# Kernel tuning notes

Measured on AMD Instinct MI355X. Metric: run time of the kernel, lower is better.

## Reference

```python
import jax, jax.numpy as jnp
import numpy as np

D = 2048
H = 16
HD = D // H
B = 2
T = 2048
EPS = 1e-5


def _gated(x, W, b, Wg, bg):
    # MoEGatedLinear: linear output elementwise-gated by sigmoid of a linear router
    return (x @ W.T + b) * jax.nn.sigmoid(x @ Wg.T + bg)


def _ln(x, g, b):
    m = jnp.mean(x, axis=-1, keepdims=True)
    v = jnp.mean((x - m) ** 2, axis=-1, keepdims=True)
    return (x - m) * jax.lax.rsqrt(v + EPS) * g + b


def setup_inputs() -> dict:
    key = jax.random.key(0)
    ks = jax.random.split(key, 16)
    w = lambda k, o, i: (jax.random.normal(k, (o, i), jnp.float32) * 0.02)
    inp = {"x": jax.random.normal(ks[0], (B, T, D), jnp.float32)}
    for i, n in enumerate(["q", "k", "v", "o"]):
        inp[f"W_{n}"] = w(jax.random.fold_in(ks[1], i), D, D)
        inp[f"b_{n}"] = jnp.zeros((D,), jnp.float32)
        inp[f"Wg_{n}"] = w(jax.random.fold_in(ks[2], i), D, D)
        inp[f"bg_{n}"] = jnp.zeros((D,), jnp.float32)
    inp["W_in"] = w(ks[3], 4 * D, D)
    inp["b_in"] = jnp.zeros((4 * D,), jnp.float32)
    inp["Wg_in"] = w(ks[4], 4 * D, D)
    inp["bg_in"] = jnp.zeros((4 * D,), jnp.float32)
    inp["W_out"] = w(ks[5], D, 4 * D)
    inp["b_out"] = jnp.zeros((D,), jnp.float32)
    inp["Wg_out"] = w(ks[6], D, 4 * D)
    inp["bg_out"] = jnp.zeros((D,), jnp.float32)
    inp["ln1_g"] = jnp.ones((D,), jnp.float32)
    inp["ln1_b"] = jnp.zeros((D,), jnp.float32)
    inp["ln2_g"] = jnp.ones((D,), jnp.float32)
    inp["ln2_b"] = jnp.zeros((D,), jnp.float32)
    return inp


def reference(x, W_q, b_q, Wg_q, bg_q, W_k, b_k, Wg_k, bg_k, W_v, b_v, Wg_v, bg_v,
              W_o, b_o, Wg_o, bg_o, W_in, b_in, Wg_in, bg_in, W_out, b_out, Wg_out, bg_out,
              ln1_g, ln1_b, ln2_g, ln2_b):
    Bb, Tt, C = x.shape
    resid = x
    h = _ln(x, ln1_g, ln1_b)
    q = _gated(h, W_q, b_q, Wg_q, bg_q).reshape(Bb, Tt, H, HD).transpose(0, 2, 1, 3)
    k = _gated(h, W_k, b_k, Wg_k, bg_k).reshape(Bb, Tt, H, HD).transpose(0, 2, 1, 3)
    v = _gated(h, W_v, b_v, Wg_v, bg_v).reshape(Bb, Tt, H, HD).transpose(0, 2, 1, 3)
    att = jnp.einsum('bhqd,bhkd->bhqk', q, k) * (1.0 / np.sqrt(HD))
    att = jax.nn.softmax(att, axis=-1)  # full (no causal mask) per source
    y = jnp.einsum('bhqk,bhkd->bhqd', att, v)
    y = y.transpose(0, 2, 1, 3).reshape(Bb, Tt, C)
    y = _gated(y, W_o, b_o, Wg_o, bg_o)
    x = resid + y
    resid = x
    h = _ln(x, ln2_g, ln2_b)
    h = _gated(h, W_in, b_in, Wg_in, bg_in)
    h = jax.nn.gelu(h, approximate=False)  # torch nn.GELU default = exact erf
    h = _gated(h, W_out, b_out, Wg_out, bg_out)
    return resid + h
```

## Files before the change

kernel.cpp:

```cpp
#include <hip/hip_runtime.h>
#include <cstdint>
#include <cmath>

#define DD 2048
#define TT 2048
#define HH 16
#define HDD 128
#define MROWS 4096

typedef __attribute__((ext_vector_type(8))) short s16x8;
typedef __attribute__((ext_vector_type(4))) float f32x4;

typedef const __attribute__((address_space(1))) void gvoid;
typedef __attribute__((address_space(3))) void lvoid;

__device__ __forceinline__ void async_cp16(const void* g, void* l) {
    __builtin_amdgcn_global_load_lds((gvoid*)g, (lvoid*)l, 16, 0, 0);
}

__device__ __forceinline__ unsigned short f2bf(float f) {
    unsigned int u = __float_as_uint(f);
    u += 0x7fffu + ((u >> 16) & 1u);
    return (unsigned short)(u >> 16);
}

__device__ __forceinline__ void store4bf(unsigned short* p, float a, float b, float c, float d) {
    union { unsigned short u[4]; uint2 v; } x;
    x.u[0] = f2bf(a); x.u[1] = f2bf(b); x.u[2] = f2bf(c); x.u[3] = f2bf(d);
    *(uint2*)p = x.v;
}

__global__ __launch_bounds__(256) void cvt_bf16(const float* __restrict__ src,
                                                unsigned short* __restrict__ dst, int n4) {
    int i = blockIdx.x * 256 + threadIdx.x;
    if (i < n4) {
        float4 v = ((const float4*)src)[i];
        store4bf(dst + (size_t)i * 4, v.x, v.y, v.z, v.w);
    }
}

__global__ __launch_bounds__(256) void ln_bf16(const float* __restrict__ x,
                                               const float* __restrict__ gg,
                                               const float* __restrict__ bb,
                                               unsigned short* __restrict__ out) {
    __shared__ float red[8];
    const int row = blockIdx.x, t = threadIdx.x;
    const float* xr = x + (size_t)row * DD;
    float4 a = ((const float4*)xr)[t];
    float4 c = ((const float4*)xr)[t + 256];
    float s = a.x + a.y + a.z + a.w + c.x + c.y + c.z + c.w;
    float q = a.x*a.x + a.y*a.y + a.z*a.z + a.w*a.w + c.x*c.x + c.y*c.y + c.z*c.z + c.w*c.w;
    #pragma unroll
    for (int m = 1; m < 64; m <<= 1) { s += __shfl_xor(s, m); q += __shfl_xor(q, m); }
    if ((t & 63) == 0) { red[t >> 6] = s; red[4 + (t >> 6)] = q; }
    __syncthreads();
    s = red[0] + red[1] + red[2] + red[3];
    q = red[4] + red[5] + red[6] + red[7];
    float mean = s * (1.f / DD);
    float var = q * (1.f / DD) - mean * mean;
    float rstd = rsqrtf(var + 1e-5f);
    float4 g1 = ((const float4*)gg)[t], b1 = ((const float4*)bb)[t];
    float4 g2 = ((const float4*)gg)[t + 256], b2 = ((const float4*)bb)[t + 256];
    unsigned short* orow = out + (size_t)row * DD;
    store4bf(orow + 4 * t,
             (a.x - mean) * rstd * g1.x + b1.x, (a.y - mean) * rstd * g1.y + b1.y,
             (a.z - mean) * rstd * g1.z + b1.z, (a.w - mean) * rstd * g1.w + b1.w);
    store4bf(orow + 1024 + 4 * t,
             (c.x - mean) * rstd * g2.x + b2.x, (c.y - mean) * rstd * g2.y + b2.y,
             (c.z - mean) * rstd * g2.z + b2.z, (c.w - mean) * rstd * g2.w + b2.w);
}

template <int EPI>
__global__ __launch_bounds__(256, 3) void gemm_gated(
        const unsigned short* __restrict__ A, const unsigned short* __restrict__ W,
        const unsigned short* __restrict__ Wg, const float* __restrict__ bias,
        const float* __restrict__ biasg, const float* __restrict__ resid,
        void* __restrict__ outp, int M, int N, int K) {
    __shared__ unsigned short lds_[(EPI == 1) ? 8704 : 8192];
    const int t = threadIdx.x, lane = t & 63, wv = t >> 6;

    const int nbg = gridDim.x;
    int pid = blockIdx.y * nbg + blockIdx.x;
    int npg = 8 * nbg;
    int grp = pid / npg;
    int loc = pid - grp * npg;
    const int m0 = (grp * 8 + (loc & 7)) * 128;
    const int n0 = (loc >> 3) * 64;

    const int srow = t >> 2;
    const int scol = (t & 3) * 8;
    const unsigned short* gA = A + (size_t)(m0 + srow) * K + scol;
    const unsigned short* gB = W + (size_t)(n0 + srow) * K + scol;
    const unsigned short* gBg = Wg + (size_t)(n0 + srow) * K + scol;

    const int mw = (wv >> 1) * 64, nw = (wv & 1) * 32;
    const int fr = lane & 15, fg = lane >> 4, fk = fg * 8;

    f32x4 zero4 = {0.f, 0.f, 0.f, 0.f};
    f32x4 acc[4][2], accg[4][2];
    #pragma unroll
    for (int i = 0; i < 4; i++)
        #pragma unroll
        for (int j = 0; j < 2; j++) { acc[i][j] = zero4; accg[i][j] = zero4; }

    for (int k0 = 0; k0 < K; k0 += 32) {
        async_cp16(gA + k0, lds_ + t * 8);
        async_cp16(gA + (size_t)64 * K + k0, lds_ + 2048 + t * 8);
        async_cp16(gB + k0, lds_ + 4096 + t * 8);
        async_cp16(gBg + k0, lds_ + 6144 + t * 8);
        __syncthreads();
        s16x8 af[4], bf_[2], bg_[2];
        #pragma unroll
        for (int i = 0; i < 4; i++)
            af[i] = *(const s16x8*)(lds_ + (mw + i * 16 + fr) * 32 + fk);
        #pragma unroll
        for (int j = 0; j < 2; j++) {
            bf_[j] = *(const s16x8*)(lds_ + 4096 + (nw + j * 16 + fr) * 32 + fk);
            bg_[j] = *(const s16x8*)(lds_ + 6144 + (nw + j * 16 + fr) * 32 + fk);
        }
        #pragma unroll
        for (int i = 0; i < 4; i++)
            #pragma unroll
            for (int j = 0; j < 2; j++) {
                acc[i][j] = __builtin_amdgcn_mfma_f32_16x16x32_bf16(af[i], bf_[j], acc[i][j], 0, 0, 0);
                accg[i][j] = __builtin_amdgcn_mfma_f32_16x16x32_bf16(af[i], bg_[j], accg[i][j], 0, 0, 0);
            }
        __syncthreads();
    }

    #pragma unroll
    for (int i = 0; i < 4; i++)
        #pragma unroll
        for (int j = 0; j < 2; j++) {
            const int n = n0 + nw + j * 16 + fr;
            const float bn = bias[n], bgn = biasg[n];
            #pragma unroll
            for (int r = 0; r < 4; r++) {
                const int m = m0 + mw + i * 16 + fg * 4 + r;
                float lin = acc[i][j][r] + bn;
                float gt = accg[i][j][r] + bgn;
                float gv = lin / (1.f + __expf(-gt));
                if constexpr (EPI == 0) {
                    ((unsigned short*)outp)[(size_t)m * N + n] = f2bf(gv);
                } else if constexpr (EPI == 1) {
                    lds_[(nw + j * 16 + fr) * 136 + (mw + i * 16 + fg * 4 + r)] = f2bf(gv);
                } else if constexpr (EPI == 2) {
                    ((float*)outp)[(size_t)m * N + n] = resid[(size_t)m * N + n] + gv;
                } else {
                    float ge = 0.5f * gv * (1.f + erff(gv * 0.70710678118f));
                    ((unsigned short*)outp)[(size_t)m * N + n] = f2bf(ge);
                }
            }
        }

    if constexpr (EPI == 1) {
        __syncthreads();
        const int n_l = t >> 2;
        const int ch = t & 3;
        const unsigned short* src = lds_ + n_l * 136 + ch * 32;
        const int hglob = n0 + n_l;
        const int b_ = m0 >> 11;
        const int tseq = (m0 & 2047) + ch * 32;
        unsigned short* dst = (unsigned short*)outp +
            (((size_t)b_ * HH + (hglob >> 7)) * HDD + (hglob & 127)) * TT + tseq;
        #pragma unroll
        for (int c = 0; c < 4; c++)
            *(uint4*)(dst + c * 8) = *(const uint4*)(src + c * 8);
    }
}

__global__ __launch_bounds__(256, 4) void attn_flash2(const unsigned short* __restrict__ Q,
                                                      const unsigned short* __restrict__ Kb,
                                                      const unsigned short* __restrict__ VT,
                                                      unsigned short* __restrict__ Y) {
    __shared__ unsigned short sK[64 * 128];
    __shared__ unsigned short sV[128 * 64];
    __shared__ unsigned short sP[4 * 1024];
    const int t = threadIdx.x, lane = t & 63, wv = t >> 6;
    const int bx = blockIdx.x;
    const int qblk = bx & 31;
    const int h = (bx >> 5) & 15;
    const int b = bx >> 9;
    const int q0 = qblk * 64 + wv * 16;
    const int fr = lane & 15, fg = lane >> 4;

    s16x8 qf[4];
    const unsigned short* qbase = Q + ((size_t)(b * TT + q0 + fr)) * DD + h * HDD + fg * 8;
    #pragma unroll
    for (int s = 0; s < 4; s++) qf[s] = *(const s16x8*)(qbase + s * 32);

    const unsigned short* kSrc[4];
    const unsigned short* vSrc[4];
    #pragma unroll
    for (int r = 0; r < 4; r++) {
        int R = r * 16 + (t >> 4);
        int c = (t & 15) ^ ((t >> 4) & 15);
        kSrc[r] = Kb + (size_t)(b * TT + R) * DD + h * HDD + c * 8;
        int hd = r * 32 + (t >> 3);
        int cv = (t & 7) ^ ((t >> 3) & 7);
        vSrc[r] = VT + ((size_t)((b * HH + h) * HDD + hd)) * TT + cv * 8;
    }
    unsigned short* sPw = sP + wv * 1024;

    f32x4 zero4 = {0.f, 0.f, 0.f, 0.f};
    f32x4 o[8];
    #pragma unroll
    for (int jo = 0; jo < 8; jo++) o[jo] = zero4;
    float Mx[4], L[4];
    #pragma unroll
    for (int r = 0; r < 4; r++) { Mx[r] = -1e30f; L[r] = 0.f; }
    const float scale = 0.08838834764831845f;

    for (int tk0 = 0; tk0 < TT; tk0 += 64) {
        #pragma unroll
        for (int r = 0; r < 4; r++) {
            async_cp16(kSrc[r] + (size_t)tk0 * DD, sK + r * 2048 + t * 8);
            async_cp16(vSrc[r] + tk0, sV + r * 2048 + t * 8);
        }
        __syncthreads();

        f32x4 sac[4];
        #pragma unroll
        for (int j = 0; j < 4; j++) sac[j] = zero4;
        #pragma unroll
        for (int j = 0; j < 4; j++)
            #pragma unroll
            for (int s = 0; s < 4; s++) {
                s16x8 kf = *(const s16x8*)(sK + (j * 16 + fr) * 128 + (((s * 4 + fg) ^ fr) * 8));
                sac[j] = __builtin_amdgcn_mfma_f32_16x16x32_bf16(qf[s], kf, sac[j], 0, 0, 0);
            }

        float alpha[4];
        #pragma unroll
        for (int j = 0; j < 4; j++)
            #pragma unroll
            for (int r = 0; r < 4; r++) sac[j][r] *= scale;
        #pragma unroll
        for (int r = 0; r < 4; r++) {
            float mx = fmaxf(fmaxf(sac[0][r], sac[1][r]), fmaxf(sac[2][r], sac[3][r]));
            mx = fmaxf(mx, __shfl_xor(mx, 1));
            mx = fmaxf(mx, __shfl_xor(mx, 2));
            mx = fmaxf(mx, __shfl_xor(mx, 4));
            mx = fmaxf(mx, __shfl_xor(mx, 8));
            float mnew = fmaxf(Mx[r], mx);
            alpha[r] = __expf(Mx[r] - mnew);
            Mx[r] = mnew;
        }
        float rs[4] = {0.f, 0.f, 0.f, 0.f};
        #pragma unroll
        for (int j = 0; j < 4; j++)
            #pragma unroll
            for (int r = 0; r < 4; r++) {
                float p = __expf(sac[j][r] - Mx[r]);
                rs[r] += p;
                int qr = fg * 4 + r;
                int cc = (j * 2 + (fr >> 3)) ^ (qr & 7);
                sPw[qr * 64 + cc * 8 + (fr & 7)] = f2bf(p);
            }
        #pragma unroll
        for (int r = 0; r < 4; r++) {
            float tsum = rs[r];
            tsum += __shfl_xor(tsum, 1);
            tsum += __shfl_xor(tsum, 2);
            tsum += __shfl_xor(tsum, 4);
            tsum += __shfl_xor(tsum, 8);
            L[r] = L[r] * alpha[r] + tsum;
        }
        #pragma unroll
        for (int jo = 0; jo < 8; jo++)
            #pragma unroll
            for (int r = 0; r < 4; r++) o[jo][r] *= alpha[r];

        s16x8 pa[2];
        #pragma unroll
        for (int ks = 0; ks < 2; ks++)
            pa[ks] = *(const s16x8*)(sPw + fr * 64 + (((ks * 4 + fg) ^ (fr & 7)) * 8));
        #pragma unroll
        for (int jo = 0; jo < 8; jo++)
            #pragma unroll
            for (int ks = 0; ks < 2; ks++) {
                s16x8 vf = *(const s16x8*)(sV + (jo * 16 + fr) * 64 + (((ks * 4 + fg) ^ (fr & 7)) * 8));
                o[jo] = __builtin_amdgcn_mfma_f32_16x16x32_bf16(pa[ks], vf, o[jo], 0, 0, 0);
            }
        __syncthreads();
    }
    float Linv[4];
    #pragma unroll
    for (int r = 0; r < 4; r++) Linv[r] = 1.f / L[r];
    #pragma unroll
    for (int jo = 0; jo < 8; jo++)
        #pragma unroll
        for (int r = 0; r < 4; r++) {
            float val = o[jo][r] * Linv[r];
            Y[((size_t)(b * TT + q0 + fg * 4 + r)) * DD + h * HDD + jo * 16 + fr] = f2bf(val);
        }
}

extern "C" void kernel_launch(void* const* d_in, const int* in_sizes, int n_in,
                              void* d_out, int out_size, void* d_ws, size_t ws_size,
                              hipStream_t stream) {
    const float* x = (const float*)d_in[0];
    auto F = [&](int i) { return (const float*)d_in[i]; };
    char* ws = (char*)d_ws;
    const size_t MB = 1ull << 20;

    static const int widx_[12] = {1, 3, 5, 7, 9, 11, 13, 15, 17, 19, 21, 23};
    static const size_t woffMB[12] = {0, 8, 16, 24, 32, 40, 48, 56, 64, 96, 128, 160};
    unsigned short* wbf[12];
    for (int i = 0; i < 12; i++) {
        wbf[i] = (unsigned short*)(ws + woffMB[i] * MB);
        size_t n = (i < 8) ? (size_t)DD * DD : (size_t)4 * DD * DD;
        cvt_bf16<<<dim3((unsigned)(n / 4 / 256)), dim3(256), 0, stream>>>(F(widx_[i]), wbf[i], (int)(n / 4));
    }
    unsigned short* hbf = (unsigned short*)(ws + 192 * MB);
    unsigned short* qb  = (unsigned short*)(ws + 208 * MB);
    unsigned short* kb  = (unsigned short*)(ws + 224 * MB);
    unsigned short* vtb = (unsigned short*)(ws + 240 * MB);
    unsigned short* yb  = (unsigned short*)(ws + 256 * MB);
    unsigned short* ub  = (unsigned short*)(ws + 208 * MB);
    float* x1 = (float*)(ws + 272 * MB);

    ln_bf16<<<dim3(MROWS), dim3(256), 0, stream>>>(x, F(25), F(26), hbf);

    dim3 blk(256);
    gemm_gated<0><<<dim3(32, 32), blk, 0, stream>>>(hbf, wbf[0], wbf[1], F(2), F(4), nullptr, qb, MROWS, DD, DD);
    gemm_gated<0><<<dim3(32, 32), blk, 0, stream>>>(hbf, wbf[2], wbf[3], F(6), F(8), nullptr, kb, MROWS, DD, DD);
    gemm_gated<1><<<dim3(32, 32), blk, 0, stream>>>(hbf, wbf[4], wbf[5], F(10), F(12), nullptr, vtb, MROWS, DD, DD);

    attn_flash2<<<dim3(1024), blk, 0, stream>>>(qb, kb, vtb, yb);

    gemm_gated<2><<<dim3(32, 32), blk, 0, stream>>>(yb, wbf[6], wbf[7], F(14), F(16), x, x1, MROWS, DD, DD);

    ln_bf16<<<dim3(MROWS), dim3(256), 0, stream>>>(x1, F(27), F(28), hbf);

    gemm_gated<3><<<dim3(128, 32), blk, 0, stream>>>(hbf, wbf[8], wbf[9], F(18), F(20), nullptr, ub, MROWS, 4 * DD, DD);
    gemm_gated<2><<<dim3(32, 32), blk, 0, stream>>>(ub, wbf[10], wbf[11], F(22), F(24), x1, (float*)d_out, MROWS, DD, 4 * DD);
}
```

Measured before the change: 1.690 ms.

## Replace gated GEMM with 256x256 interleaved-weight pipelined 8-wave kernel

Weights W and Wg are interleaved in 16-row blocks during bf16 conversion, so a single B operand tile holds both the linear and the gate columns. The GEMM moves from 128x64 tiles with 256 threads to 256x256 tiles with 512 threads. It uses double-buffered 64-wide K steps in a swizzled LDS layout, split-phase loads overlapped with MFMA, setprio, and explicit vmcnt waits. The aim is higher arithmetic intensity and better latency hiding. The trade-offs are heavy register and LDS use (128KB LDS, occupancy 2) and fewer workgroups, which can leave CUs underfilled on the 2048-wide GEMMs (256 blocks).

```diff
diff --git a/kernel.cpp b/kernel.cpp
--- a/kernel.cpp
+++ b/kernel.cpp
@@ -30,13 +30,16 @@
     *(uint2*)p = x.v;
 }
 
-__global__ __launch_bounds__(256) void cvt_bf16(const float* __restrict__ src,
-                                                unsigned short* __restrict__ dst, int n4) {
-    int i = blockIdx.x * 256 + threadIdx.x;
-    if (i < n4) {
-        float4 v = ((const float4*)src)[i];
-        store4bf(dst + (size_t)i * 4, v.x, v.y, v.z, v.w);
-    }
+__global__ __launch_bounds__(256) void cvt_ilv(const float* __restrict__ W,
+                                               const float* __restrict__ Wg,
+                                               unsigned short* __restrict__ out, int k4shift) {
+    int g = blockIdx.x * 256 + threadIdx.x;
+    int rp = g >> k4shift;
+    int c4 = g & ((1 << k4shift) - 1);
+    int jb = rp >> 5, s = rp & 15, sel = (rp >> 4) & 1;
+    const float* src = (sel ? Wg : W) + (((size_t)(jb * 16 + s)) << (k4shift + 2)) + c4 * 4;
+    float4 v = *(const float4*)src;
+    store4bf(out + (((size_t)rp) << (k4shift + 2)) + c4 * 4, v.x, v.y, v.z, v.w);
 }
 
 __global__ __launch_bounds__(256) void ln_bf16(const float* __restrict__ x,
@@ -70,102 +73,181 @@
              (c.z - mean) * rstd * g2.z + b2.z, (c.w - mean) * rstd * g2.w + b2.w);
 }
 
+#define G8_LDA(base, iq) do { \
+    _Pragma("unroll") \
+    for (int i2_ = 0; i2_ < 4; i2_++) \
+        af[i2_] = *(const s16x8*)(lds + (base) + aRd + ((iq) * 4 + i2_) * 1024); \
+} while (0)
+#define G8_LDB(base) do { \
+    _Pragma("unroll") \
+    for (int j_ = 0; j_ < 4; j_++) \
+        bf[j_] = *(const s16x8*)(lds + (base) + bRd + j_ * 1024); \
+} while (0)
+#define G8_MMA(iq) do { \
+    __builtin_amdgcn_s_setprio(1); \
+    _Pragma("unroll") \
+    for (int i2_ = 0; i2_ < 4; i2_++) { \
+        _Pragma("unroll") \
+        for (int j_ = 0; j_ < 4; j_++) \
+            acc[(iq) * 4 + i2_][j_] = __builtin_amdgcn_mfma_f32_16x16x32_bf16( \
+                af[i2_], bf[j_], acc[(iq) * 4 + i2_][j_], 0, 0, 0); \
+    } \
+    __builtin_amdgcn_s_setprio(0); \
+} while (0)
+#define G8_BAR() __builtin_amdgcn_s_barrier()
+#define G8_SCB() __builtin_amdgcn_sched_barrier(0)
+#define G8_VM4() asm volatile("s_waitcnt vmcnt(4)" ::: "memory")
+#define G8_VM0() asm volatile("s_waitcnt vmcnt(0)" ::: "memory")
+
 template <int EPI>
-__global__ __launch_bounds__(256, 3) void gemm_gated(
-        const unsigned short* __restrict__ A, const unsigned short* __restrict__ W,
-        const unsigned short* __restrict__ Wg, const float* __restrict__ bias,
-        const float* __restrict__ biasg, const float* __restrict__ resid,
-        void* __restrict__ outp, int M, int N, int K) {
-    __shared__ unsigned short lds_[(EPI == 1) ? 8704 : 8192];
+__global__ __launch_bounds__(512, 2) void gemm_gated8(
+        const unsigned short* __restrict__ A, const unsigned short* __restrict__ Wi,
+        const float* __restrict__ bias, const float* __restrict__ biasg,
+        const float* __restrict__ resid, void* __restrict__ outp,
+        int M, int Ntrue, int K) {
+    __shared__ unsigned short lds_[65536];
+    char* lds = (char*)lds_;
     const int t = threadIdx.x, lane = t & 63, wv = t >> 6;
-
-    const int nbg = gridDim.x;
-    int pid = blockIdx.y * nbg + blockIdx.x;
-    int npg = 8 * nbg;
-    int grp = pid / npg;
-    int loc = pid - grp * npg;
-    const int m0 = (grp * 8 + (loc & 7)) * 128;
-    const int n0 = (loc >> 3) * 64;
-
-    const int srow = t >> 2;
-    const int scol = (t & 3) * 8;
-    const unsigned short* gA = A + (size_t)(m0 + srow) * K + scol;
-    const unsigned short* gB = W + (size_t)(n0 + srow) * K + scol;
-    const unsigned short* gBg = Wg + (size_t)(n0 + srow) * K + scol;
-
-    const int mw = (wv >> 1) * 64, nw = (wv & 1) * 32;
-    const int fr = lane & 15, fg = lane >> 4, fk = fg * 8;
-
+    const int fr = lane & 15, fg = lane >> 4;
+    const int wr = wv >> 2, wc = wv & 3;
+
+    const int nM = M >> 8;
+    const int nwg = gridDim.x;
+    const int pid = blockIdx.x;
+    const int swz = (pid & 7) * (nwg >> 3) + (pid >> 3);
+    const int nt = swz / nM;
+    const int mt = swz - nt * nM;
+    const int m0 = mt << 8;
+    const int np0 = nt << 8;
+
+    const unsigned short* aP[2];
+    const unsigned short* bP[2];
+    int ldst[2];
+    #pragma unroll
+    for (int l = 0; l < 2; l++) {
+        int idx = l * 512 + t;
+        int p = idx >> 3, pc = idx & 7;
+        int spc = pc ^ (p & 7);
+        int lr = 2 * p + (spc >> 2);
+        int ke = (spc & 3) * 8;
+        aP[l] = A + (size_t)(m0 + lr) * K + ke;
+        bP[l] = Wi + (size_t)(np0 + lr) * K + ke;
+        ldst[l] = idx * 16;
+    }
+    const int chR = (((fr & 1) << 2) | fg) ^ ((fr >> 1) & 7);
+    const int aRd = (wr * 64 + (fr >> 1)) * 128 + chR * 16;
+    const int bRd = (wc * 32 + (fr >> 1)) * 128 + chR * 16;
+
+    f32x4 acc[8][4];
     f32x4 zero4 = {0.f, 0.f, 0.f, 0.f};
-    f32x4 acc[4][2], accg[4][2];
-    #pragma unroll
-    for (int i = 0; i < 4; i++)
-        #pragma unroll
-        for (int j = 0; j < 2; j++) { acc[i][j] = zero4; accg[i][j] = zero4; }
-
-    for (int k0 = 0; k0 < K; k0 += 32) {
-        async_cp16(gA + k0, lds_ + t * 8);
-        async_cp16(gA + (size_t)64 * K + k0, lds_ + 2048 + t * 8);
-        async_cp16(gB + k0, lds_ + 4096 + t * 8);
-        async_cp16(gBg + k0, lds_ + 6144 + t * 8);
-        __syncthreads();
-        s16x8 af[4], bf_[2], bg_[2];
-        #pragma unroll
-        for (int i = 0; i < 4; i++)
-            af[i] = *(const s16x8*)(lds_ + (mw + i * 16 + fr) * 32 + fk);
-        #pragma unroll
-        for (int j = 0; j < 2; j++) {
-            bf_[j] = *(const s16x8*)(lds_ + 4096 + (nw + j * 16 + fr) * 32 + fk);
-            bg_[j] = *(const s16x8*)(lds_ + 6144 + (nw + j * 16 + fr) * 32 + fk);
-        }
-        #pragma unroll
-        for (int i = 0; i < 4; i++)
-            #pragma unroll
-            for (int j = 0; j < 2; j++) {
-                acc[i][j] = __builtin_amdgcn_mfma_f32_16x16x32_bf16(af[i], bf_[j], acc[i][j], 0, 0, 0);
-                accg[i][j] = __builtin_amdgcn_mfma_f32_16x16x32_bf16(af[i], bg_[j], accg[i][j], 0, 0, 0);
+    #pragma unroll
+    for (int i = 0; i < 8; i++)
+        #pragma unroll
+        for (int j = 0; j < 4; j++) acc[i][j] = zero4;
+    s16x8 af[4], bf[4];
+
+    async_cp16(aP[0], lds + ldst[0]);
+    async_cp16(aP[1], lds + ldst[1]);
+    async_cp16(bP[0], lds + 65536 + ldst[0]);
+    async_cp16(bP[1], lds + 65536 + ldst[1]);
+    async_cp16(aP[0] + 32, lds + 16384 + ldst[0]);
+    async_cp16(aP[1] + 32, lds + 16384 + ldst[1]);
+    async_cp16(bP[0] + 32, lds + 65536 + 16384 + ldst[0]);
+    async_cp16(bP[1] + 32, lds + 65536 + 16384 + ldst[1]);
+    G8_VM4(); G8_BAR(); G8_SCB();
+
+    const int NT = K >> 6;
+    for (int kt = 0; kt < NT - 1; kt++) {
+        const int sA = (kt & 1) << 15;
+        const int sB = 65536 + sA;
+        const int nAb = sA ^ 32768;
+        const int nBb = 65536 + nAb;
+        const int kn = (kt + 1) << 6;
+        G8_LDA(sA, 0); G8_LDB(sB);
+        async_cp16(aP[0] + kn, lds + nAb + ldst[0]);
+        async_cp16(aP[1] + kn, lds + nAb + ldst[1]);
+        G8_BAR();
+        G8_MMA(0);
+        G8_BAR();
+        G8_LDA(sA, 1);
+        async_cp16(bP[0] + kn, lds + nBb + ldst[0]);
+        async_cp16(bP[1] + kn, lds + nBb + ldst[1]);
+        G8_VM4(); G8_BAR(); G8_SCB();
+        G8_MMA(1);
+        G8_BAR();
+        G8_LDA(sA + 16384, 0); G8_LDB(sB + 16384);
+        async_cp16(aP[0] + kn + 32, lds + nAb + 16384 + ldst[0]);
+        async_cp16(aP[1] + kn + 32, lds + nAb + 16384 + ldst[1]);
+        G8_BAR();
+        G8_MMA(0);
+        G8_BAR();
+        G8_LDA(sA + 16384, 1);
+        async_cp16(bP[0] + kn + 32, lds + nBb + 16384 + ldst[0]);
+        async_cp16(bP[1] + kn + 32, lds + nBb + 16384 + ldst[1]);
+        G8_VM4(); G8_BAR(); G8_SCB();
+        G8_MMA(1);
+        G8_BAR();
+    }
+    {
+        const int sA = ((NT - 1) & 1) << 15;
+        const int sB = 65536 + sA;
+        G8_LDA(sA, 0); G8_LDB(sB);
+        G8_BAR(); G8_MMA(0); G8_BAR();
+        G8_LDA(sA, 1);
+        G8_VM0(); G8_BAR(); G8_SCB();
+        G8_MMA(1); G8_BAR();
+        G8_LDA(sA + 16384, 0); G8_LDB(sB + 16384);
+        G8_BAR(); G8_MMA(0); G8_BAR();
+        G8_LDA(sA + 16384, 1);
+        G8_MMA(1);
+    }
+
+    const int mB = m0 + wr * 128 + fg * 4;
+    const int nB = (nt << 7) + wc * 32 + fr;
+    if constexpr (EPI == 1) {
+        const int b_ = m0 >> 11;
+        unsigned short* vt = (unsigned short*)outp;
+        #pragma unroll
+        for (int i = 0; i < 8; i++)
+            #pragma unroll
+            for (int jp = 0; jp < 2; jp++) {
+                const int n = nB + jp * 16;
+                const float bn = bias[n], bgn = biasg[n];
+                float g4[4];
+                #pragma unroll
+                for (int r = 0; r < 4; r++) {
+                    float lin = acc[i][2 * jp][r] + bn;
+                    float gt = acc[i][2 * jp + 1][r] + bgn;
+                    g4[r] = lin / (1.f + __expf(-gt));
+                }
+                unsigned short* dst = vt + ((size_t)b_ * 2048 + n) * 2048 +
+                                      (m0 & 2047) + wr * 128 + i * 16 + fg * 4;
+                store4bf(dst, g4[0], g4[1], g4[2], g4[3]);
             }
-        __syncthreads();
-    }
-
-    #pragma unroll
-    for (int i = 0; i < 4; i++)
-        #pragma unroll
-        for (int j = 0; j < 2; j++) {
-            const int n = n0 + nw + j * 16 + fr;
-            const float bn = bias[n], bgn = biasg[n];
-            #pragma unroll
-            for (int r = 0; r < 4; r++) {
-                const int m = m0 + mw + i * 16 + fg * 4 + r;
-                float lin = acc[i][j][r] + bn;
-                float gt = accg[i][j][r] + bgn;
-                float gv = lin / (1.f + __expf(-gt));
-                if constexpr (EPI == 0) {
-                    ((unsigned short*)outp)[(size_t)m * N + n] = f2bf(gv);
-                } else if constexpr (EPI == 1) {
-                    lds_[(nw + j * 16 + fr) * 136 + (mw + i * 16 + fg * 4 + r)] = f2bf(gv);
-                } else if constexpr (EPI == 2) {
-                    ((float*)outp)[(size_t)m * N + n] = resid[(size_t)m * N + n] + gv;
-                } else {
-                    float ge = 0.5f * gv * (1.f + erff(gv * 0.70710678118f));
-                    ((unsigned short*)outp)[(size_t)m * N + n] = f2bf(ge);
+    } else {
+        #pragma unroll
+        for (int i = 0; i < 8; i++)
+            #pragma unroll
+            for (int jp = 0; jp < 2; jp++) {
+                const int n = nB + jp * 16;
+                const float bn = bias[n], bgn = biasg[n];
+                #pragma unroll
+                for (int r = 0; r < 4; r++) {
+                    const int m = mB + i * 16 + r;
+                    float lin = acc[i][2 * jp][r] + bn;
+                    float gt = acc[i][2 * jp + 1][r] + bgn;
+                    float gv = lin / (1.f + __expf(-gt));
+                    if constexpr (EPI == 0) {
+                        ((unsigned short*)outp)[(size_t)m * Ntrue + n] = f2bf(gv);
+                    } else if constexpr (EPI == 2) {
+                        ((float*)outp)[(size_t)m * Ntrue + n] =
+                            resid[(size_t)m * Ntrue + n] + gv;
+                    } else {
+                        float ge = 0.5f * gv * (1.f + erff(gv * 0.70710678118f));
+                        ((unsigned short*)outp)[(size_t)m * Ntrue + n] = f2bf(ge);
+                    }
                 }
             }
-        }
-
-    if constexpr (EPI == 1) {
-        __syncthreads();
-        const int n_l = t >> 2;
-        const int ch = t & 3;
-        const unsigned short* src = lds_ + n_l * 136 + ch * 32;
-        const int hglob = n0 + n_l;
-        const int b_ = m0 >> 11;
-        const int tseq = (m0 & 2047) + ch * 32;
-        unsigned short* dst = (unsigned short*)outp +
-            (((size_t)b_ * HH + (hglob >> 7)) * HDD + (hglob & 127)) * TT + tseq;
-        #pragma unroll
-        for (int c = 0; c < 4; c++)
-            *(uint4*)(dst + c * 8) = *(const uint4*)(src + c * 8);
     }
 }
 
@@ -304,14 +386,19 @@
     char* ws = (char*)d_ws;
     const size_t MB = 1ull << 20;
 
-    static const int widx_[12] = {1, 3, 5, 7, 9, 11, 13, 15, 17, 19, 21, 23};
-    static const size_t woffMB[12] = {0, 8, 16, 24, 32, 40, 48, 56, 64, 96, 128, 160};
-    unsigned short* wbf[12];
-    for (int i = 0; i < 12; i++) {
-        wbf[i] = (unsigned short*)(ws + woffMB[i] * MB);
-        size_t n = (i < 8) ? (size_t)DD * DD : (size_t)4 * DD * DD;
-        cvt_bf16<<<dim3((unsigned)(n / 4 / 256)), dim3(256), 0, stream>>>(F(widx_[i]), wbf[i], (int)(n / 4));
-    }
+    unsigned short* wi_q  = (unsigned short*)(ws + 0 * MB);
+    unsigned short* wi_k  = (unsigned short*)(ws + 16 * MB);
+    unsigned short* wi_v  = (unsigned short*)(ws + 32 * MB);
+    unsigned short* wi_o  = (unsigned short*)(ws + 48 * MB);
+    unsigned short* wi_in = (unsigned short*)(ws + 64 * MB);
+    unsigned short* wi_ot = (unsigned short*)(ws + 128 * MB);
+    cvt_ilv<<<dim3(8192), dim3(256), 0, stream>>>(F(1), F(3), wi_q, 9);
+    cvt_ilv<<<dim3(8192), dim3(256), 0, stream>>>(F(5), F(7), wi_k, 9);
+    cvt_ilv<<<dim3(8192), dim3(256), 0, stream>>>(F(9), F(11), wi_v, 9);
+    cvt_ilv<<<dim3(8192), dim3(256), 0, stream>>>(F(13), F(15), wi_o, 9);
+    cvt_ilv<<<dim3(32768), dim3(256), 0, stream>>>(F(17), F(19), wi_in, 9);
+    cvt_ilv<<<dim3(32768), dim3(256), 0, stream>>>(F(21), F(23), wi_ot, 11);
+
     unsigned short* hbf = (unsigned short*)(ws + 192 * MB);
     unsigned short* qb  = (unsigned short*)(ws + 208 * MB);
     unsigned short* kb  = (unsigned short*)(ws + 224 * MB);
@@ -322,17 +409,17 @@
 
     ln_bf16<<<dim3(MROWS), dim3(256), 0, stream>>>(x, F(25), F(26), hbf);
 
-    dim3 blk(256);
-    gemm_gated<0><<<dim3(32, 32), blk, 0, stream>>>(hbf, wbf[0], wbf[1], F(2), F(4), nullptr, qb, MROWS, DD, DD);
-    gemm_gated<0><<<dim3(32, 32), blk, 0, stream>>>(hbf, wbf[2], wbf[3], F(6), F(8), nullptr, kb, MROWS, DD, DD);
-    gemm_gated<1><<<dim3(32, 32), blk, 0, stream>>>(hbf, wbf[4], wbf[5], F(10), F(12), nullptr, vtb, MROWS, DD, DD);
-
-    attn_flash2<<<dim3(1024), blk, 0, stream>>>(qb, kb, vtb, yb);
-
-    gemm_gated<2><<<dim3(32, 32), blk, 0, stream>>>(yb, wbf[6], wbf[7], F(14), F(16), x, x1, MROWS, DD, DD);
+    dim3 blk(512);
+    gemm_gated8<0><<<dim3(256), blk, 0, stream>>>(hbf, wi_q, F(2), F(4), nullptr, qb, MROWS, DD, DD);
+    gemm_gated8<0><<<dim3(256), blk, 0, stream>>>(hbf, wi_k, F(6), F(8), nullptr, kb, MROWS, DD, DD);
+    gemm_gated8<1><<<dim3(256), blk, 0, stream>>>(hbf, wi_v, F(10), F(12), nullptr, vtb, MROWS, DD, DD);
+
+    attn_flash2<<<dim3(1024), dim3(256), 0, stream>>>(qb, kb, vtb, yb);
+
+    gemm_gated8<2><<<dim3(256), blk, 0, stream>>>(yb, wi_o, F(14), F(16), x, x1, MROWS, DD, DD);
 
     ln_bf16<<<dim3(MROWS), dim3(256), 0, stream>>>(x1, F(27), F(28), hbf);
 
-    gemm_gated<3><<<dim3(128, 32), blk, 0, stream>>>(hbf, wbf[8], wbf[9], F(18), F(20), nullptr, ub, MROWS, 4 * DD, DD);
-    gemm_gated<2><<<dim3(32, 32), blk, 0, stream>>>(ub, wbf[10], wbf[11], F(22), F(24), x1, (float*)d_out, MROWS, DD, 4 * DD);
-}
+    gemm_gated8<3><<<dim3(1024), blk, 0, stream>>>(hbf, wi_in, F(18), F(20), nullptr, ub, MROWS, 4 * DD, DD);
+    gemm_gated8<2><<<dim3(256), blk, 0, stream>>>(ub, wi_ot, F(22), F(24), x1, (float*)d_out, MROWS, DD, 4 * DD);
+}
```

New measurement: 1.403 ms. -17.0%, faster.
